# Optimization experiments

Measured on AMD Instinct MI355X. Metric: run time of the kernel, lower is better.

Reference implementation:

```python
import jax, jax.numpy as jnp
import numpy as np

N_NODES = 100000
N_EDGES = 1600000
D_FEAT = 128
HIDDEN = 16
N_CLASSES = 16


def setup_inputs() -> dict:
    key = jax.random.key(0)
    ks = jax.random.split(key, 6)
    x = jax.random.normal(ks[0], (N_NODES, D_FEAT), dtype=jnp.float32)
    edge_index = jax.random.randint(ks[1], (2, N_EDGES), 0, N_NODES, dtype=jnp.int64)
    # Glorot-ish scaled weights
    w1_rel = jax.random.normal(ks[2], (D_FEAT, HIDDEN), dtype=jnp.float32) / np.sqrt(D_FEAT)
    w1_root = jax.random.normal(ks[3], (D_FEAT, HIDDEN), dtype=jnp.float32) / np.sqrt(D_FEAT)
    b1 = jnp.zeros((HIDDEN,), dtype=jnp.float32)
    w2_rel = jax.random.normal(ks[4], (HIDDEN, N_CLASSES), dtype=jnp.float32) / np.sqrt(HIDDEN)
    w2_root = jax.random.normal(ks[5], (HIDDEN, N_CLASSES), dtype=jnp.float32) / np.sqrt(HIDDEN)
    b2 = jnp.zeros((N_CLASSES,), dtype=jnp.float32)
    return {"x": x, "edge_index": edge_index, "w1_rel": w1_rel, "w1_root": w1_root,
            "b1": b1, "w2_rel": w2_rel, "w2_root": w2_root, "b2": b2}


def _graph_conv(x, src, dst, w_rel, w_root, b):
    # PyG GraphConv(aggr='add'): out_i = lin_rel(sum_{j->i} x_j) + lin_root(x_i)
    n = x.shape[0]
    agg = jax.ops.segment_sum(x[src], dst, num_segments=n)  # [N, d_in]
    return agg @ w_rel + x @ w_root + b


def reference(x, edge_index, w1_rel, w1_root, b1, w2_rel, w2_root, b2):
    src, dst = edge_index[0], edge_index[1]
    h = jax.nn.relu(_graph_conv(x, src, dst, w1_rel, w1_root, b1))
    # F.dropout(training=False) -> identity in eval mode
    out = _graph_conv(h, src, dst, w2_rel, w2_root, b2)
    return jax.nn.log_softmax(out, axis=1)
```

## Files before the change

### kernel.cpp

```cpp
#include <hip/hip_runtime.h>

#define DFEAT 128
#define HID 16
#define BKT_NODES 128
#define BKT_SHIFT 7
#define CAP 2432
#define CAPI 5
#define CHUNK 8192
#define NOEDGE 0xFFFFFFFFu

typedef __attribute__((ext_vector_type(8))) short short8;
typedef __attribute__((ext_vector_type(4))) float floatx4;

__device__ __forceinline__ float bf2f(unsigned v) { return __uint_as_float(v << 16); }
__device__ __forceinline__ unsigned short f2bf(float f) {
    unsigned u = __float_as_uint(f);
    return (unsigned short)((u + 0x7FFFu + ((u >> 16) & 1u)) >> 16);
}
__device__ __forceinline__ unsigned pack2(float a, float b) {
    return (unsigned)f2bf(a) | ((unsigned)f2bf(b) << 16);
}

__global__ __launch_bounds__(512) void k_detect(const unsigned short* __restrict__ x,
                                                const int* __restrict__ ei,
                                                int* __restrict__ flags,
                                                int* __restrict__ gcur, int nbkt) {
    const int t = threadIdx.x;
    for (int i = t; i < nbkt; i += 512) gcur[i] = 0;
    if (t < 64) {
        unsigned short v = x[2 * t];
        int e = (v >> 7) & 0xFF;
        bool okbf = (v == 0) || (e >= 110 && e <= 130);
        unsigned long long mbf = __ballot(okbf);
        bool z = (ei[2 * t + 1] == 0);
        unsigned long long mz = __ballot(z);
        if (t == 0) {
            flags[0] = (__popcll(mbf) >= 52) ? 1 : 0;
            flags[1] = (__popcll(mz) >= 60) ? 1 : 0;
        }
    }
}

__global__ __launch_bounds__(512) void k_pl(const int* __restrict__ ei,
                                            unsigned* __restrict__ eb,
                                            int* __restrict__ gcur,
                                            const void* __restrict__ xv,
                                            const void* __restrict__ wrel,
                                            const void* __restrict__ wroot,
                                            unsigned short* __restrict__ p1b,
                                            unsigned short* __restrict__ q1b,
                                            const int* __restrict__ flags,
                                            int E, int nbkt, int N, int nPart) {
    __shared__ int hist[1024];
    const int t = threadIdx.x;

    if ((int)blockIdx.x < nPart) {
        for (int i = t; i < nbkt; i += 512) hist[i] = 0;
        __syncthreads();
        const int base = blockIdx.x * CHUNK;
        const int i64 = flags[1];
        unsigned pk[16];
        unsigned short bk[16];
        if (i64 && !(E & 1)) {
#pragma unroll
            for (int ip = 0; ip < 8; ++ip) {
                int e = base + ip * 1024 + 2 * t;
                if (e < E) {
                    int4 sv = *(const int4*)(ei + 2 * (size_t)e);
                    int4 dv = *(const int4*)(ei + 2 * ((size_t)E + e));
                    int b0 = dv.x >> BKT_SHIFT;
                    pk[2 * ip] = ((unsigned)sv.x << BKT_SHIFT) | (unsigned)(dv.x & (BKT_NODES - 1));
                    bk[2 * ip] = (unsigned short)b0;
                    atomicAdd(&hist[b0], 1);
                    int b1 = dv.z >> BKT_SHIFT;
                    pk[2 * ip + 1] = ((unsigned)sv.z << BKT_SHIFT) | (unsigned)(dv.z & (BKT_NODES - 1));
                    bk[2 * ip + 1] = (unsigned short)b1;
                    atomicAdd(&hist[b1], 1);
                } else {
                    bk[2 * ip] = 0xFFFFu;
                    bk[2 * ip + 1] = 0xFFFFu;
                }
            }
        } else {
#pragma unroll
            for (int i = 0; i < 16; ++i) {
                int e = base + i * 512 + t;
                if (e < E) {
                    int src, dst;
                    if (i64) { src = ei[2 * (size_t)e]; dst = ei[2 * ((size_t)E + e)]; }
                    else     { src = ei[e];             dst = ei[(size_t)E + e]; }
                    int b = dst >> BKT_SHIFT;
                    pk[i] = ((unsigned)src << BKT_SHIFT) | (unsigned)(dst & (BKT_NODES - 1));
                    bk[i] = (unsigned short)b;
                    atomicAdd(&hist[b], 1);
                } else {
                    bk[i] = 0xFFFFu;
                }
            }
        }
        __syncthreads();
        for (int b = t; b < nbkt; b += 512) {
            int c = hist[b];
            hist[b] = c ? atomicAdd(&gcur[b], c) : 0;
        }
        __syncthreads();
#pragma unroll
        for (int i = 0; i < 16; ++i) {
            if (bk[i] != 0xFFFFu) {
                int pos = atomicAdd(&hist[bk[i]], 1);
                if (pos >= 0 && pos < CAP)
                    eb[(size_t)bk[i] * CAP + pos] = pk[i];
            }
        }
        return;
    }

    const int lane = t & 63, wave = t >> 6;
    const int bf = flags[0];
    const int m = lane & 15;
    const int quad = lane >> 4;
    const int nodebase = ((int)blockIdx.x - nPart) * 128 + wave * 16;

    short8 Brel[4], Broot[4];
    if (bf) {
        const unsigned short* a = (const unsigned short*)wrel;
        const unsigned short* c = (const unsigned short*)wroot;
#pragma unroll
        for (int kb = 0; kb < 4; ++kb) {
            short8 br, bo;
#pragma unroll
            for (int j = 0; j < 8; ++j) {
                int k = kb * 32 + quad * 8 + j;
                br[j] = (short)a[k * HID + m];
                bo[j] = (short)c[k * HID + m];
            }
            Brel[kb] = br; Broot[kb] = bo;
        }
    } else {
        const float* a = (const float*)wrel;
        const float* c = (const float*)wroot;
#pragma unroll
        for (int kb = 0; kb < 4; ++kb) {
            short8 br, bo;
#pragma unroll
            for (int j = 0; j < 8; ++j) {
                int k = kb * 32 + quad * 8 + j;
                br[j] = (short)f2bf(a[k * HID + m]);
                bo[j] = (short)f2bf(c[k * HID + m]);
            }
            Brel[kb] = br; Broot[kb] = bo;
        }
    }

    int row = nodebase + m;
    if (row >= N) row = N - 1;

    floatx4 accP = {0.f, 0.f, 0.f, 0.f}, accQ = {0.f, 0.f, 0.f, 0.f};
    if (bf) {
        const unsigned short* xp = (const unsigned short*)xv;
        const unsigned short* rp = xp + (size_t)row * DFEAT + quad * 8;
#pragma unroll
        for (int kb = 0; kb < 4; ++kb) {
            short8 A = *(const short8*)(rp + kb * 32);
            accP = __builtin_amdgcn_mfma_f32_16x16x32_bf16(A, Brel[kb], accP, 0, 0, 0);
            accQ = __builtin_amdgcn_mfma_f32_16x16x32_bf16(A, Broot[kb], accQ, 0, 0, 0);
        }
    } else {
        const float* xp = (const float*)xv;
        const float* rp = xp + (size_t)row * DFEAT + quad * 8;
#pragma unroll
        for (int kb = 0; kb < 4; ++kb) {
            float4 v0 = *(const float4*)(rp + kb * 32);
            float4 v1 = *(const float4*)(rp + kb * 32 + 4);
            short8 A;
            A[0] = (short)f2bf(v0.x); A[1] = (short)f2bf(v0.y);
            A[2] = (short)f2bf(v0.z); A[3] = (short)f2bf(v0.w);
            A[4] = (short)f2bf(v1.x); A[5] = (short)f2bf(v1.y);
            A[6] = (short)f2bf(v1.z); A[7] = (short)f2bf(v1.w);
            accP = __builtin_amdgcn_mfma_f32_16x16x32_bf16(A, Brel[kb], accP, 0, 0, 0);
            accQ = __builtin_amdgcn_mfma_f32_16x16x32_bf16(A, Broot[kb], accQ, 0, 0, 0);
        }
    }

#pragma unroll
    for (int r = 0; r < 4; ++r) {
        int node = nodebase + quad * 4 + r;
        if (node < N) {
            p1b[(size_t)node * HID + m] = f2bf(accP[r]);
            q1b[(size_t)node * HID + m] = f2bf(accQ[r]);
        }
    }
}

__global__ __launch_bounds__(512) void k_sagg1(const unsigned* __restrict__ eb,
                                               const int* __restrict__ gcur,
                                               const unsigned short* __restrict__ p1b,
                                               const unsigned short* __restrict__ q1b,
                                               const void* __restrict__ b1,
                                               const void* __restrict__ w2rel,
                                               const void* __restrict__ w2root,
                                               unsigned short* __restrict__ p2b,
                                               unsigned short* __restrict__ q2b,
                                               unsigned* __restrict__ csr,
                                               int* __restrict__ offsets,
                                               int* __restrict__ ends,
                                               const int* __restrict__ flags,
                                               int N) {
    __shared__ unsigned srt[CAP];
    __shared__ int cnts[BKT_NODES];
    __shared__ int offs[BKT_NODES];
    __shared__ float4 swp[HID][8];
    __shared__ float sb[HID];
    const int t = threadIdx.x;
    const int b = blockIdx.x;
    const int bf = flags[0];

    if (t < 128) {
        int k = t >> 3, p = t & 7;
        float4 w;
        if (bf) {
            const unsigned short* a = (const unsigned short*)w2rel;
            const unsigned short* c = (const unsigned short*)w2root;
            w = make_float4(bf2f(a[k * 16 + 2 * p]), bf2f(a[k * 16 + 2 * p + 1]),
                            bf2f(c[k * 16 + 2 * p]), bf2f(c[k * 16 + 2 * p + 1]));
        } else {
            const float* a = (const float*)w2rel;
            const float* c = (const float*)w2root;
            w = make_float4(a[k * 16 + 2 * p], a[k * 16 + 2 * p + 1],
                            c[k * 16 + 2 * p], c[k * 16 + 2 * p + 1]);
        }
        swp[k][p] = w;
    }
    if (t < HID) sb[t] = bf ? bf2f(((const unsigned short*)b1)[t]) : ((const float*)b1)[t];
    if (t < BKT_NODES) cnts[t] = 0;
    __syncthreads();

    int cnt = gcur[b];
    if (cnt < 0) cnt = 0;
    if (cnt > CAP) cnt = CAP;
    const unsigned* ep = eb + (size_t)b * CAP;

    unsigned ev[CAPI];
    int rk[CAPI];
#pragma unroll
    for (int i = 0; i < CAPI; ++i) {
        int e = i * 512 + t;
        if (e < cnt) {
            unsigned w = ep[e];
            ev[i] = w;
            rk[i] = atomicAdd(&cnts[w & (BKT_NODES - 1u)], 1);
        } else ev[i] = NOEDGE;
    }
    __syncthreads();
    if (t < BKT_NODES) offs[t] = cnts[t];
    __syncthreads();
    for (int off = 1; off < BKT_NODES; off <<= 1) {
        int v = 0;
        if (t >= off && t < BKT_NODES) v = offs[t - off];
        __syncthreads();
        if (t < BKT_NODES) offs[t] += v;
        __syncthreads();
    }
#pragma unroll
    for (int i = 0; i < CAPI; ++i) {
        if (ev[i] != NOEDGE) {
            unsigned local = ev[i] & (BKT_NODES - 1u);
            int pos = offs[local] - cnts[local] + rk[i];
            srt[pos] = ev[i] >> BKT_SHIFT;
        }
    }
    __syncthreads();

    const int base = b * CAP;
    for (int e = t; e < cnt; e += 512) csr[base + e] = srt[e];
    const int gb = b * BKT_NODES;
    if (t < BKT_NODES) {
        int gn = gb + t;
        if (gn < N) {
            offsets[gn] = base + offs[t] - cnts[t];
            ends[gn]    = base + offs[t];
        }
    }

    const int grp = t >> 3, jp = t & 7;
#pragma unroll
    for (int g = 0; g < 2; ++g) {
        int node = g * 64 + grp;
        int gn = gb + node;
        int beg = offs[node] - cnts[node];
        int end = offs[node];
        float2 acc = make_float2(0.f, 0.f);
        int e = beg;
        for (; e + 4 <= end; e += 4) {
            unsigned s0 = srt[e], s1 = srt[e + 1], s2 = srt[e + 2], s3 = srt[e + 3];
            unsigned u0 = *(const unsigned*)(p1b + (size_t)s0 * HID + 2 * jp);
            unsigned u1 = *(const unsigned*)(p1b + (size_t)s1 * HID + 2 * jp);
            unsigned u2 = *(const unsigned*)(p1b + (size_t)s2 * HID + 2 * jp);
            unsigned u3 = *(const unsigned*)(p1b + (size_t)s3 * HID + 2 * jp);
            acc.x += bf2f(u0 & 0xFFFFu) + bf2f(u1 & 0xFFFFu)
                   + bf2f(u2 & 0xFFFFu) + bf2f(u3 & 0xFFFFu);
            acc.y += bf2f(u0 >> 16) + bf2f(u1 >> 16) + bf2f(u2 >> 16) + bf2f(u3 >> 16);
        }
        for (; e < end; ++e) {
            unsigned u = *(const unsigned*)(p1b + (size_t)srt[e] * HID + 2 * jp);
            acc.x += bf2f(u & 0xFFFFu);
            acc.y += bf2f(u >> 16);
        }
        float hx = 0.f, hy = 0.f;
        if (gn < N) {
            unsigned qu = *(const unsigned*)(q1b + (size_t)gn * HID + 2 * jp);
            hx = fmaxf(acc.x + bf2f(qu & 0xFFFFu) + sb[2 * jp], 0.f);
            hy = fmaxf(acc.y + bf2f(qu >> 16) + sb[2 * jp + 1], 0.f);
        }
        float2 sp = make_float2(0.f, 0.f), sq = make_float2(0.f, 0.f);
#pragma unroll
        for (int k = 0; k < HID; ++k) {
            float hsel = (k & 1) ? hy : hx;
            float hk = __shfl(hsel, k >> 1, 8);
            float4 w = swp[k][jp];
            sp.x += hk * w.x; sp.y += hk * w.y;
            sq.x += hk * w.z; sq.y += hk * w.w;
        }
        if (gn < N) {
            ((unsigned*)p2b)[(size_t)gn * 8 + jp] = pack2(sp.x, sp.y);
            ((unsigned*)q2b)[(size_t)gn * 8 + jp] = pack2(sq.x, sq.y);
        }
    }
}

__global__ __launch_bounds__(256) void k_agg2(const int* __restrict__ offsets,
                                              const int* __restrict__ ends,
                                              const unsigned* __restrict__ csr,
                                              const unsigned short* __restrict__ p2b,
                                              const unsigned short* __restrict__ q2b,
                                              const void* __restrict__ b2,
                                              void* __restrict__ out,
                                              const int* __restrict__ flags,
                                              int N) {
    __shared__ float sb[HID];
    const int t = threadIdx.x;
    const int bf = flags[0];
    if (t < HID) sb[t] = bf ? bf2f(((const unsigned short*)b2)[t]) : ((const float*)b2)[t];
    __syncthreads();

    const int grp = t >> 3, jp = t & 7;
    const int n = blockIdx.x * 32 + grp;
    if (n >= N) return;

    const int beg = offsets[n], end = ends[n];
    float2 acc = make_float2(0.f, 0.f);
    int e = beg;
    for (; e + 8 <= end; e += 8) {
        unsigned s0 = csr[e],     s1 = csr[e + 1], s2 = csr[e + 2], s3 = csr[e + 3];
        unsigned s4 = csr[e + 4], s5 = csr[e + 5], s6 = csr[e + 6], s7 = csr[e + 7];
        unsigned u0 = *(const unsigned*)(p2b + (size_t)s0 * HID + 2 * jp);
        unsigned u1 = *(const unsigned*)(p2b + (size_t)s1 * HID + 2 * jp);
        unsigned u2 = *(const unsigned*)(p2b + (size_t)s2 * HID + 2 * jp);
        unsigned u3 = *(const unsigned*)(p2b + (size_t)s3 * HID + 2 * jp);
        unsigned u4 = *(const unsigned*)(p2b + (size_t)s4 * HID + 2 * jp);
        unsigned u5 = *(const unsigned*)(p2b + (size_t)s5 * HID + 2 * jp);
        unsigned u6 = *(const unsigned*)(p2b + (size_t)s6 * HID + 2 * jp);
        unsigned u7 = *(const unsigned*)(p2b + (size_t)s7 * HID + 2 * jp);
        acc.x += bf2f(u0 & 0xFFFFu) + bf2f(u1 & 0xFFFFu)
               + bf2f(u2 & 0xFFFFu) + bf2f(u3 & 0xFFFFu)
               + bf2f(u4 & 0xFFFFu) + bf2f(u5 & 0xFFFFu)
               + bf2f(u6 & 0xFFFFu) + bf2f(u7 & 0xFFFFu);
        acc.y += bf2f(u0 >> 16) + bf2f(u1 >> 16) + bf2f(u2 >> 16) + bf2f(u3 >> 16)
               + bf2f(u4 >> 16) + bf2f(u5 >> 16) + bf2f(u6 >> 16) + bf2f(u7 >> 16);
    }
    for (; e + 2 <= end; e += 2) {
        unsigned s0 = csr[e], s1 = csr[e + 1];
        unsigned u0 = *(const unsigned*)(p2b + (size_t)s0 * HID + 2 * jp);
        unsigned u1 = *(const unsigned*)(p2b + (size_t)s1 * HID + 2 * jp);
        acc.x += bf2f(u0 & 0xFFFFu) + bf2f(u1 & 0xFFFFu);
        acc.y += bf2f(u0 >> 16) + bf2f(u1 >> 16);
    }
    for (; e < end; ++e) {
        unsigned u = *(const unsigned*)(p2b + (size_t)csr[e] * HID + 2 * jp);
        acc.x += bf2f(u & 0xFFFFu);
        acc.y += bf2f(u >> 16);
    }
    unsigned qu = *(const unsigned*)(q2b + (size_t)n * HID + 2 * jp);
    float ox = acc.x + bf2f(qu & 0xFFFFu) + sb[2 * jp];
    float oy = acc.y + bf2f(qu >> 16) + sb[2 * jp + 1];

    float m = fmaxf(ox, oy);
#pragma unroll
    for (int mask = 1; mask < 8; mask <<= 1) m = fmaxf(m, __shfl_xor(m, mask, 8));
    float s = __expf(ox - m) + __expf(oy - m);
#pragma unroll
    for (int mask = 1; mask < 8; mask <<= 1) s += __shfl_xor(s, mask, 8);
    const float l = m + __logf(s);

    if (bf) ((unsigned*)out)[(size_t)n * 8 + jp] = pack2(ox - l, oy - l);
    else    ((float2*)out)[(size_t)n * 8 + jp] = make_float2(ox - l, oy - l);
}

extern "C" void kernel_launch(void* const* d_in, const int* in_sizes, int n_in,
                              void* d_out, int out_size, void* d_ws, size_t ws_size,
                              hipStream_t stream) {
    const void* x       = d_in[0];
    const int*  ei      = (const int*)d_in[1];
    const void* w1_rel  = d_in[2];
    const void* w1_root = d_in[3];
    const void* b1      = d_in[4];
    const void* w2_rel  = d_in[5];
    const void* w2_root = d_in[6];
    const void* b2      = d_in[7];

    const int N = in_sizes[0] / DFEAT;
    const int E = in_sizes[1] / 2;
    const int nbkt = (N + BKT_NODES - 1) / BKT_NODES;

    unsigned short* p1b = (unsigned short*)d_ws;
    unsigned short* q1b = p1b + (size_t)N * HID;
    unsigned short* p2b = q1b + (size_t)N * HID;
    unsigned short* q2b = p2b + (size_t)N * HID;
    unsigned* eb   = (unsigned*)(q2b + (size_t)N * HID);
    unsigned* csr  = eb + (size_t)nbkt * CAP;
    int* offsets   = (int*)(csr + (size_t)nbkt * CAP);
    int* ends      = offsets + N;
    int* gcur      = ends + N;
    int* flags     = gcur + nbkt;

    const int nPart = (E + CHUNK - 1) / CHUNK;
    const int nLin  = (N + 127) / 128;

    k_detect<<<1, 512, 0, stream>>>((const unsigned short*)x, ei, flags, gcur, nbkt);
    k_pl<<<nPart + nLin, 512, 0, stream>>>(ei, eb, gcur, x, w1_rel, w1_root,
                                           p1b, q1b, flags, E, nbkt, N, nPart);
    k_sagg1<<<nbkt, 512, 0, stream>>>(eb, gcur, p1b, q1b, b1, w2_rel, w2_root,
                                      p2b, q2b, csr, offsets, ends, flags, N);
    k_agg2<<<(N + 31) / 32, 256, 0, stream>>>(offsets, ends, csr, p2b, q2b, b2,
                                              d_out, flags, N);
}
```

Measured before the change: 158.5 us.

## Record bucket ranks during histogram and stage bucket CSR in LDS for layer-2 aggregation

In partitioning, each edge keeps the rank returned by its first shared-memory atomicAdd, packed with its bucket index, so the scatter step needs no second atomic per edge. The layer-2 aggregation kernel now runs one 512-thread block per 128-node bucket. Each block copies that bucket's CSR slice into shared memory and takes node ends from the next offset or the bucket count, which removes the separate ends array. This cuts LDS atomics and global reads of CSR indices, but layer 2 now launches far fewer, larger blocks, which may hurt latency hiding.

```diff
diff --git a/kernel.cpp b/kernel.cpp
--- a/kernel.cpp
+++ b/kernel.cpp
@@ -60,7 +60,7 @@
         const int base = blockIdx.x * CHUNK;
         const int i64 = flags[1];
         unsigned pk[16];
-        unsigned short bk[16];
+        unsigned bkrk[16];
         if (i64 && !(E & 1)) {
 #pragma unroll
             for (int ip = 0; ip < 8; ++ip) {
@@ -70,15 +70,15 @@
                     int4 dv = *(const int4*)(ei + 2 * ((size_t)E + e));
                     int b0 = dv.x >> BKT_SHIFT;
                     pk[2 * ip] = ((unsigned)sv.x << BKT_SHIFT) | (unsigned)(dv.x & (BKT_NODES - 1));
-                    bk[2 * ip] = (unsigned short)b0;
-                    atomicAdd(&hist[b0], 1);
+                    int r0 = atomicAdd(&hist[b0], 1);
+                    bkrk[2 * ip] = ((unsigned)b0 << 13) | (unsigned)r0;
                     int b1 = dv.z >> BKT_SHIFT;
                     pk[2 * ip + 1] = ((unsigned)sv.z << BKT_SHIFT) | (unsigned)(dv.z & (BKT_NODES - 1));
-                    bk[2 * ip + 1] = (unsigned short)b1;
-                    atomicAdd(&hist[b1], 1);
+                    int r1 = atomicAdd(&hist[b1], 1);
+                    bkrk[2 * ip + 1] = ((unsigned)b1 << 13) | (unsigned)r1;
                 } else {
-                    bk[2 * ip] = 0xFFFFu;
-                    bk[2 * ip + 1] = 0xFFFFu;
+                    bkrk[2 * ip] = NOEDGE;
+                    bkrk[2 * ip + 1] = NOEDGE;
                 }
             }
         } else {
@@ -91,10 +91,10 @@
                     else     { src = ei[e];             dst = ei[(size_t)E + e]; }
                     int b = dst >> BKT_SHIFT;
                     pk[i] = ((unsigned)src << BKT_SHIFT) | (unsigned)(dst & (BKT_NODES - 1));
-                    bk[i] = (unsigned short)b;
-                    atomicAdd(&hist[b], 1);
+                    int r = atomicAdd(&hist[b], 1);
+                    bkrk[i] = ((unsigned)b << 13) | (unsigned)r;
                 } else {
-                    bk[i] = 0xFFFFu;
+                    bkrk[i] = NOEDGE;
                 }
             }
         }
@@ -106,10 +106,11 @@
         __syncthreads();
 #pragma unroll
         for (int i = 0; i < 16; ++i) {
-            if (bk[i] != 0xFFFFu) {
-                int pos = atomicAdd(&hist[bk[i]], 1);
-                if (pos >= 0 && pos < CAP)
-                    eb[(size_t)bk[i] * CAP + pos] = pk[i];
+            if (bkrk[i] != NOEDGE) {
+                int b = (int)(bkrk[i] >> 13);
+                int pos = hist[b] + (int)(bkrk[i] & 0x1FFFu);
+                if (pos < CAP)
+                    eb[(size_t)b * CAP + pos] = pk[i];
             }
         }
         return;
@@ -203,7 +204,6 @@
                                                unsigned short* __restrict__ q2b,
                                                unsigned* __restrict__ csr,
                                                int* __restrict__ offsets,
-                                               int* __restrict__ ends,
                                                const int* __restrict__ flags,
                                                int N) {
     __shared__ unsigned srt[CAP];
@@ -276,10 +276,7 @@
     const int gb = b * BKT_NODES;
     if (t < BKT_NODES) {
         int gn = gb + t;
-        if (gn < N) {
-            offsets[gn] = base + offs[t] - cnts[t];
-            ends[gn]    = base + offs[t];
-        }
+        if (gn < N) offsets[gn] = base + offs[t] - cnts[t];
     }
 
     const int grp = t >> 3, jp = t & 7;
@@ -328,8 +325,8 @@
     }
 }
 
-__global__ __launch_bounds__(256) void k_agg2(const int* __restrict__ offsets,
-                                              const int* __restrict__ ends,
+__global__ __launch_bounds__(512) void k_agg2(const int* __restrict__ offsets,
+                                              const int* __restrict__ gcur,
                                               const unsigned* __restrict__ csr,
                                               const unsigned short* __restrict__ p2b,
                                               const unsigned short* __restrict__ q2b,
@@ -337,63 +334,81 @@
                                               void* __restrict__ out,
                                               const int* __restrict__ flags,
                                               int N) {
+    __shared__ unsigned srt[CAP];
     __shared__ float sb[HID];
     const int t = threadIdx.x;
+    const int b = blockIdx.x;
     const int bf = flags[0];
     if (t < HID) sb[t] = bf ? bf2f(((const unsigned short*)b2)[t]) : ((const float*)b2)[t];
+
+    int cnt = gcur[b];
+    if (cnt < 0) cnt = 0;
+    if (cnt > CAP) cnt = CAP;
+    const int base = b * CAP;
+    for (int e = t; e < cnt; e += 512) srt[e] = csr[base + e];
     __syncthreads();
 
+    const int gb = b * BKT_NODES;
     const int grp = t >> 3, jp = t & 7;
-    const int n = blockIdx.x * 32 + grp;
-    if (n >= N) return;
-
-    const int beg = offsets[n], end = ends[n];
-    float2 acc = make_float2(0.f, 0.f);
-    int e = beg;
-    for (; e + 8 <= end; e += 8) {
-        unsigned s0 = csr[e],     s1 = csr[e + 1], s2 = csr[e + 2], s3 = csr[e + 3];
-        unsigned s4 = csr[e + 4], s5 = csr[e + 5], s6 = csr[e + 6], s7 = csr[e + 7];
-        unsigned u0 = *(const unsigned*)(p2b + (size_t)s0 * HID + 2 * jp);
-        unsigned u1 = *(const unsigned*)(p2b + (size_t)s1 * HID + 2 * jp);
-        unsigned u2 = *(const unsigned*)(p2b + (size_t)s2 * HID + 2 * jp);
-        unsigned u3 = *(const unsigned*)(p2b + (size_t)s3 * HID + 2 * jp);
-        unsigned u4 = *(const unsigned*)(p2b + (size_t)s4 * HID + 2 * jp);
-        unsigned u5 = *(const unsigned*)(p2b + (size_t)s5 * HID + 2 * jp);
-        unsigned u6 = *(const unsigned*)(p2b + (size_t)s6 * HID + 2 * jp);
-        unsigned u7 = *(const unsigned*)(p2b + (size_t)s7 * HID + 2 * jp);
-        acc.x += bf2f(u0 & 0xFFFFu) + bf2f(u1 & 0xFFFFu)
-               + bf2f(u2 & 0xFFFFu) + bf2f(u3 & 0xFFFFu)
-               + bf2f(u4 & 0xFFFFu) + bf2f(u5 & 0xFFFFu)
-               + bf2f(u6 & 0xFFFFu) + bf2f(u7 & 0xFFFFu);
-        acc.y += bf2f(u0 >> 16) + bf2f(u1 >> 16) + bf2f(u2 >> 16) + bf2f(u3 >> 16)
-               + bf2f(u4 >> 16) + bf2f(u5 >> 16) + bf2f(u6 >> 16) + bf2f(u7 >> 16);
-    }
-    for (; e + 2 <= end; e += 2) {
-        unsigned s0 = csr[e], s1 = csr[e + 1];
-        unsigned u0 = *(const unsigned*)(p2b + (size_t)s0 * HID + 2 * jp);
-        unsigned u1 = *(const unsigned*)(p2b + (size_t)s1 * HID + 2 * jp);
-        acc.x += bf2f(u0 & 0xFFFFu) + bf2f(u1 & 0xFFFFu);
-        acc.y += bf2f(u0 >> 16) + bf2f(u1 >> 16);
-    }
-    for (; e < end; ++e) {
-        unsigned u = *(const unsigned*)(p2b + (size_t)csr[e] * HID + 2 * jp);
-        acc.x += bf2f(u & 0xFFFFu);
-        acc.y += bf2f(u >> 16);
-    }
-    unsigned qu = *(const unsigned*)(q2b + (size_t)n * HID + 2 * jp);
-    float ox = acc.x + bf2f(qu & 0xFFFFu) + sb[2 * jp];
-    float oy = acc.y + bf2f(qu >> 16) + sb[2 * jp + 1];
-
-    float m = fmaxf(ox, oy);
-#pragma unroll
-    for (int mask = 1; mask < 8; mask <<= 1) m = fmaxf(m, __shfl_xor(m, mask, 8));
-    float s = __expf(ox - m) + __expf(oy - m);
-#pragma unroll
-    for (int mask = 1; mask < 8; mask <<= 1) s += __shfl_xor(s, mask, 8);
-    const float l = m + __logf(s);
-
-    if (bf) ((unsigned*)out)[(size_t)n * 8 + jp] = pack2(ox - l, oy - l);
-    else    ((float2*)out)[(size_t)n * 8 + jp] = make_float2(ox - l, oy - l);
+#pragma unroll
+    for (int g = 0; g < 2; ++g) {
+        int node = g * 64 + grp;
+        int gn = gb + node;
+        int beg = 0, end = 0;
+        if (gn < N) {
+            beg = offsets[gn] - base;
+            end = (node == BKT_NODES - 1 || gn + 1 >= N) ? cnt : offsets[gn + 1] - base;
+        }
+        float2 acc = make_float2(0.f, 0.f);
+        int e = beg;
+        for (; e + 8 <= end; e += 8) {
+            unsigned s0 = srt[e],     s1 = srt[e + 1], s2 = srt[e + 2], s3 = srt[e + 3];
+            unsigned s4 = srt[e + 4], s5 = srt[e + 5], s6 = srt[e + 6], s7 = srt[e + 7];
+            unsigned u0 = *(const unsigned*)(p2b + (size_t)s0 * HID + 2 * jp);
+            unsigned u1 = *(const unsigned*)(p2b + (size_t)s1 * HID + 2 * jp);
+            unsigned u2 = *(const unsigned*)(p2b + (size_t)s2 * HID + 2 * jp);
+            unsigned u3 = *(const unsigned*)(p2b + (size_t)s3 * HID + 2 * jp);
+            unsigned u4 = *(const unsigned*)(p2b + (size_t)s4 * HID + 2 * jp);
+            unsigned u5 = *(const unsigned*)(p2b + (size_t)s5 * HID + 2 * jp);
+            unsigned u6 = *(const unsigned*)(p2b + (size_t)s6 * HID + 2 * jp);
+            unsigned u7 = *(const unsigned*)(p2b + (size_t)s7 * HID + 2 * jp);
+            acc.x += bf2f(u0 & 0xFFFFu) + bf2f(u1 & 0xFFFFu)
+                   + bf2f(u2 & 0xFFFFu) + bf2f(u3 & 0xFFFFu)
+                   + bf2f(u4 & 0xFFFFu) + bf2f(u5 & 0xFFFFu)
+                   + bf2f(u6 & 0xFFFFu) + bf2f(u7 & 0xFFFFu);
+            acc.y += bf2f(u0 >> 16) + bf2f(u1 >> 16) + bf2f(u2 >> 16) + bf2f(u3 >> 16)
+                   + bf2f(u4 >> 16) + bf2f(u5 >> 16) + bf2f(u6 >> 16) + bf2f(u7 >> 16);
+        }
+        for (; e + 2 <= end; e += 2) {
+            unsigned s0 = srt[e], s1 = srt[e + 1];
+            unsigned u0 = *(const unsigned*)(p2b + (size_t)s0 * HID + 2 * jp);
+            unsigned u1 = *(const unsigned*)(p2b + (size_t)s1 * HID + 2 * jp);
+            acc.x += bf2f(u0 & 0xFFFFu) + bf2f(u1 & 0xFFFFu);
+            acc.y += bf2f(u0 >> 16) + bf2f(u1 >> 16);
+        }
+        for (; e < end; ++e) {
+            unsigned u = *(const unsigned*)(p2b + (size_t)srt[e] * HID + 2 * jp);
+            acc.x += bf2f(u & 0xFFFFu);
+            acc.y += bf2f(u >> 16);
+        }
+        float ox = 0.f, oy = 0.f;
+        if (gn < N) {
+            unsigned qu = *(const unsigned*)(q2b + (size_t)gn * HID + 2 * jp);
+            ox = acc.x + bf2f(qu & 0xFFFFu) + sb[2 * jp];
+            oy = acc.y + bf2f(qu >> 16) + sb[2 * jp + 1];
+        }
+        float m = fmaxf(ox, oy);
+#pragma unroll
+        for (int mask = 1; mask < 8; mask <<= 1) m = fmaxf(m, __shfl_xor(m, mask, 8));
+        float s = __expf(ox - m) + __expf(oy - m);
+#pragma unroll
+        for (int mask = 1; mask < 8; mask <<= 1) s += __shfl_xor(s, mask, 8);
+        const float l = m + __logf(s);
+        if (gn < N) {
+            if (bf) ((unsigned*)out)[(size_t)gn * 8 + jp] = pack2(ox - l, oy - l);
+            else    ((float2*)out)[(size_t)gn * 8 + jp] = make_float2(ox - l, oy - l);
+        }
+    }
 }
 
 extern "C" void kernel_launch(void* const* d_in, const int* in_sizes, int n_in,
@@ -419,8 +434,7 @@
     unsigned* eb   = (unsigned*)(q2b + (size_t)N * HID);
     unsigned* csr  = eb + (size_t)nbkt * CAP;
     int* offsets   = (int*)(csr + (size_t)nbkt * CAP);
-    int* ends      = offsets + N;
-    int* gcur      = ends + N;
+    int* gcur      = offsets + N;
     int* flags     = gcur + nbkt;
 
     const int nPart = (E + CHUNK - 1) / CHUNK;
@@ -430,7 +444,7 @@
     k_pl<<<nPart + nLin, 512, 0, stream>>>(ei, eb, gcur, x, w1_rel, w1_root,
                                            p1b, q1b, flags, E, nbkt, N, nPart);
     k_sagg1<<<nbkt, 512, 0, stream>>>(eb, gcur, p1b, q1b, b1, w2_rel, w2_root,
-                                      p2b, q2b, csr, offsets, ends, flags, N);
-    k_agg2<<<(N + 31) / 32, 256, 0, stream>>>(offsets, ends, csr, p2b, q2b, b2,
-                                              d_out, flags, N);
-}
+                                      p2b, q2b, csr, offsets, flags, N);
+    k_agg2<<<nbkt, 512, 0, stream>>>(offsets, gcur, csr, p2b, q2b, b2,
+                                     d_out, flags, N);
+}
```

After: 155.2 us. 2.1% less time.
